# Optimization experiments

Hardware: AMD Instinct MI355X
Metric: run time of the kernel (lower is better)

## Reference

```python
import jax, jax.numpy as jnp
import numpy as np

B, S = 32, 128
VIDEO_SIZE, TITLE_SIZE = 768, 768
NUM_TAG, NUM_VOCAB, HIDDEN = 10000, 21128, 256


def setup_inputs() -> dict:
    key = jax.random.key(0)
    ks = jax.random.split(key, 10)
    video_feature = jax.random.normal(ks[0], (B, VIDEO_SIZE), dtype=jnp.float32)
    title_feature = jax.random.normal(ks[1], (B, S, TITLE_SIZE), dtype=jnp.float32)
    label_tag = jax.random.uniform(ks[2], (B, NUM_TAG), dtype=jnp.float32)
    label_mlm = jax.random.randint(ks[3], (B, S), 0, NUM_VOCAB, dtype=jnp.int64)
    Wt = jax.random.normal(ks[4], (NUM_TAG, VIDEO_SIZE), dtype=jnp.float32) * 0.02
    bt = jnp.zeros((NUM_TAG,), dtype=jnp.float32)
    Wm = jax.random.normal(ks[5], (NUM_VOCAB, TITLE_SIZE), dtype=jnp.float32) * 0.02
    bm = jnp.zeros((NUM_VOCAB,), dtype=jnp.float32)
    Wh = jax.random.normal(ks[6], (HIDDEN, VIDEO_SIZE + TITLE_SIZE), dtype=jnp.float32) * 0.02
    bh = jnp.zeros((HIDDEN,), dtype=jnp.float32)
    return {
        "video_feature": video_feature,
        "title_feature": title_feature,
        "label_tag": label_tag,
        "label_mlm": label_mlm,
        "Wt": Wt, "bt": bt, "Wm": Wm, "bm": bm, "Wh": Wh, "bh": bh,
    }


def reference(video_feature, title_feature, label_tag, label_mlm, Wt, bt, Wm, bm, Wh, bh):
    # tag head + BCEWithLogits (mean reduction), numerically stable form
    pred_tag = video_feature @ Wt.T + bt                       # [B, NUM_TAG]
    loss_tag = jnp.mean(
        jnp.maximum(pred_tag, 0.0) - pred_tag * label_tag
        + jnp.log1p(jnp.exp(-jnp.abs(pred_tag)))
    )
    pred_tag_sig = jax.nn.sigmoid(pred_tag)

    # mlm head: per-token vocab logits, masked CE summed over nonzero labels
    logits = jnp.einsum('bsd,vd->bsv', title_feature, Wm) + bm  # [B, S, V]
    lse = jax.nn.logsumexp(logits, axis=-1)                     # [B, S]
    gold = jnp.take_along_axis(logits, label_mlm[..., None], axis=-1)[..., 0]
    ce = lse - gold                                             # per-token NLL
    mask = (label_mlm != 0)
    loss_mlm = jnp.sum(jnp.where(mask, ce, 0.0))

    # fused embedding head + L2 normalize (torch eps 1e-12)
    feature = jnp.concatenate([video_feature, title_feature[:, 0]], axis=1)
    embedding = feature @ Wh.T + bh                             # [B, HIDDEN]
    norm = jnp.linalg.norm(embedding, axis=1, keepdims=True)
    normed_embedding = embedding / jnp.maximum(norm, 1e-12)

    return (pred_tag_sig, normed_embedding, loss_tag, loss_mlm)
```

## Files before the change

kernel.cpp:

```cpp
#include <hip/hip_runtime.h>
#include <hip/hip_bf16.h>
#include <math.h>

typedef short bf16x8 __attribute__((ext_vector_type(8)));
typedef float f32x4 __attribute__((ext_vector_type(4)));

#define KDIM 768
#define NTAG 10000
#define NVOC 21128
#define HID 256
#define NTOK 4096
#define NCHUNK 24
#define CHUNK 881
#define NTILE 56
#define M0 4.0f
#define WMSCALE 16.0f
#define INVSCALE 0.0625f
#define LOG2E 1.44269504f

#define WS_A     0ull
#define WS_AVID  3145728ull
#define WS_PSUM  3194880ull
#define WS_GOLD  3588096ull
#define WS_TAGL  3604480ull
#define WS_WM8   3604544ull
#define WS_NEED  (WS_WM8 + 16226304ull + 65536ull)

#define OUT_EMB  320000
#define OUT_LTAG 328192
#define OUT_LMLM 328193

#define TAG_BLKS 313
#define GOLD_BLKS 1024
#define EMB_BLKS 32

typedef const __attribute__((address_space(1))) unsigned int glds_g;
typedef __attribute__((address_space(3))) unsigned int glds_l;

static __device__ __forceinline__ unsigned short f2bf(float f) {
  unsigned u = __builtin_bit_cast(unsigned, f);
  u = u + 0x7FFFu + ((u >> 16) & 1u);
  return (unsigned short)(u >> 16);
}

static __device__ __forceinline__ int pk4_fp8(float4 v, float scale) {
  int w = __builtin_amdgcn_cvt_pk_fp8_f32(v.x * scale, v.y * scale, 0, false);
  w = __builtin_amdgcn_cvt_pk_fp8_f32(v.z * scale, v.w * scale, w, true);
  return w;
}

__global__ __launch_bounds__(256) void k_conv(
    const float* __restrict__ title, const float* __restrict__ video,
    const float* __restrict__ Wm,
    char* __restrict__ A8, unsigned short* __restrict__ Avid,
    char* __restrict__ Wm8, float* __restrict__ tagSum) {
  const int nT = 393216;
  const int nV = 3072;
  const int nW = 2028288;
  int i = blockIdx.x * 256 + threadIdx.x;
  if (i == 0) tagSum[0] = 0.f;
  if (i < nT) {
    float4 v0 = ((const float4*)title)[i * 2];
    float4 v1 = ((const float4*)title)[i * 2 + 1];
    int2 o = {pk4_fp8(v0, 1.f), pk4_fp8(v1, 1.f)};
    *(int2*)(A8 + (size_t)i * 8) = o;
  } else if (i < nT + nV) {
    int j = i - nT;
    float4 v0 = ((const float4*)video)[j * 2];
    float4 v1 = ((const float4*)video)[j * 2 + 1];
    bf16x8 o;
    o[0] = (short)f2bf(v0.x); o[1] = (short)f2bf(v0.y);
    o[2] = (short)f2bf(v0.z); o[3] = (short)f2bf(v0.w);
    o[4] = (short)f2bf(v1.x); o[5] = (short)f2bf(v1.y);
    o[6] = (short)f2bf(v1.z); o[7] = (short)f2bf(v1.w);
    *(bf16x8*)(Avid + (size_t)j * 8) = o;
  } else {
    int j = i - nT - nV;
    if (j >= nW) return;
    float4 v0 = ((const float4*)Wm)[j * 2];
    float4 v1 = ((const float4*)Wm)[j * 2 + 1];
    int2 o = {pk4_fp8(v0, WMSCALE), pk4_fp8(v1, WMSCALE)};
    *(int2*)(Wm8 + (size_t)j * 8) = o;
  }
}

template<bool WM8>
__global__ __launch_bounds__(256)
__attribute__((amdgpu_waves_per_eu(3, 3)))
void k_mlm(
    const char* __restrict__ A8,
    const float* __restrict__ Wm,
    const char* __restrict__ Wm8,
    const float* __restrict__ bm,
    float* __restrict__ psum) {
  __shared__ __align__(1024) char Bsm[2][12288];
  __shared__ float biasS[NTILE * 16];
  const int tid = threadIdx.x;
  const int lane = tid & 63, g = lane >> 4, col = lane & 15;
  const int wave = tid >> 6;
  const int chunk = blockIdx.x % NCHUNK, mt = blockIdx.x / NCHUNK;
  const int nbeg = chunk * CHUNK;
  const int nend = min(nbeg + CHUNK, NVOC);

  for (int i = tid; i < NTILE * 16; i += 256) {
    int n = nbeg + i;
    biasS[i] = (n < nend) ? (bm[n] - M0) * LOG2E : -1e30f;
  }

  const int arow0 = mt * 128 + wave * 32;
  long a0[24], a1[24];
  #pragma unroll
  for (int kk = 0; kk < 24; ++kk) {
    a0[kk] = *(const long*)(A8 + (size_t)(arow0 + col) * KDIM + kk * 32 + g * 8);
    a1[kk] = *(const long*)(A8 + (size_t)(arow0 + 16 + col) * KDIM + kk * 32 + g * 8);
  }

  float s[8];
  #pragma unroll
  for (int i = 0; i < 8; ++i) s[i] = 0.f;

  int e[3];
  #pragma unroll
  for (int j = 0; j < 3; ++j) {
    int sg = j * 256 + tid;
    int kk2 = sg >> 6, nl = (sg >> 2) & 15, q = sg & 3;
    int qp = q ^ ((nl >> 1) & 3);
    e[j] = nl * KDIM + kk2 * 64 + qp * 16;
  }

  const int off0 = col * 64 + ((g * 8) ^ (((col >> 1) & 3) << 4));
  const float kinv = INVSCALE * LOG2E;

  auto COMPUTE = [&](int t) {
    const char* Bb = &Bsm[t & 1][0];
    const char* B0 = Bb + off0;
    const char* B1 = Bb + (off0 ^ 32);
    f32x4 acc0 = {0.f, 0.f, 0.f, 0.f}, acc1 = {0.f, 0.f, 0.f, 0.f};
    #pragma unroll
    for (int kk = 0; kk < 24; ++kk) {
      long b = *(const long*)(((kk & 1) ? B1 : B0) + (kk >> 1) * 1024);
      acc0 = __builtin_amdgcn_mfma_f32_16x16x32_fp8_fp8(a0[kk], b, acc0, 0, 0, 0);
      acc1 = __builtin_amdgcn_mfma_f32_16x16x32_fp8_fp8(a1[kk], b, acc1, 0, 0, 0);
    }
    const float bias2 = biasS[t * 16 + col];
    #pragma unroll
    for (int rr = 0; rr < 4; ++rr) {
      s[rr]     += exp2f(fmaf(acc0[rr], kinv, bias2));
      s[rr + 4] += exp2f(fmaf(acc1[rr], kinv, bias2));
    }
  };

  if constexpr (WM8) {
    auto STAGE = [&](int buf, int tt) {
      const char* src = Wm8 + (size_t)(nbeg + tt * 16) * KDIM;
      char* dst = &Bsm[buf][0] + wave * 1024;
      #pragma unroll
      for (int j = 0; j < 3; ++j) {
        __builtin_amdgcn_global_load_lds((glds_g*)(src + e[j]),
                                         (glds_l*)(dst + j * 4096), 16, 0, 0);
      }
    };
    STAGE(0, 0);
    asm volatile("s_waitcnt lgkmcnt(0)" ::: "memory");
    __builtin_amdgcn_s_barrier();
    for (int t = 0; t < NTILE; ++t) {
      int tn = (t + 1 < NTILE) ? t + 1 : 0;
      STAGE((t + 1) & 1, tn);
      asm volatile("s_waitcnt vmcnt(3)" ::: "memory");
      __builtin_amdgcn_s_barrier();
      __builtin_amdgcn_sched_barrier(0);
      __builtin_amdgcn_s_setprio(1);
      COMPUTE(t);
      __builtin_amdgcn_s_setprio(0);
      __builtin_amdgcn_sched_barrier(0);
      __builtin_amdgcn_s_barrier();
    }
  } else {
    __syncthreads();
    for (int t = 0; t < NTILE; ++t) {
      #pragma unroll
      for (int j = 0; j < 3; ++j) {
        int sg = j * 256 + tid;
        int n = nbeg + t * 16 + ((sg >> 2) & 15);
        int kk2 = sg >> 6, q = sg & 3;
        int qp = q ^ ((((sg >> 2) & 15) >> 1) & 3);
        int koff = kk2 * 64 + qp * 16;
        int4 o = {0, 0, 0, 0};
        if (n < NVOC) {
          const float* wp = Wm + (size_t)n * KDIM + koff;
          float4 f0 = ((const float4*)wp)[0], f1 = ((const float4*)wp)[1];
          float4 f2 = ((const float4*)wp)[2], f3 = ((const float4*)wp)[3];
          o.x = pk4_fp8(f0, WMSCALE); o.y = pk4_fp8(f1, WMSCALE);
          o.z = pk4_fp8(f2, WMSCALE); o.w = pk4_fp8(f3, WMSCALE);
        }
        *(int4*)(&Bsm[0][0] + sg * 16) = o;
      }
      __syncthreads();
      COMPUTE(t);
      __syncthreads();
    }
  }

  #pragma unroll
  for (int i = 0; i < 8; ++i) {
    float v = s[i];
    v += __shfl_xor(v, 1);
    v += __shfl_xor(v, 2);
    v += __shfl_xor(v, 4);
    v += __shfl_xor(v, 8);
    s[i] = v;
  }
  if (col == 0) {
    #pragma unroll
    for (int mblk = 0; mblk < 2; ++mblk)
      #pragma unroll
      for (int rr = 0; rr < 4; ++rr) {
        int tok = arow0 + mblk * 16 + g * 4 + rr;
        psum[tok * NCHUNK + chunk] = s[mblk * 4 + rr];
      }
  }
}

__global__ __launch_bounds__(256) void k_tail(
    const unsigned short* __restrict__ Avid,
    const float* __restrict__ Wt, const float* __restrict__ bt,
    const float* __restrict__ ylab,
    const float* __restrict__ title, const int* __restrict__ lab,
    const float* __restrict__ Wm, const float* __restrict__ bm,
    const float* __restrict__ video,
    const float* __restrict__ Wh, const float* __restrict__ bh,
    float* __restrict__ out_sig, float* __restrict__ tagSum,
    float* __restrict__ gold, float* __restrict__ out_emb) {
  __shared__ __align__(1024) char smem[49664];
  const int bid = blockIdx.x, tid = threadIdx.x;
  const int wave = tid >> 6, lane = tid & 63, g = lane >> 4, col = lane & 15;

  if (bid < TAG_BLKS) {
    unsigned short* Bt = (unsigned short*)smem;
    float* wsum = (float*)(smem + 49152);
    #pragma unroll
    for (int j = 0; j < 12; ++j) {
      int sg = j * 256 + tid;
      int tt = (j >= 6) ? 1 : 0;
      int sgl = sg - tt * 1536;
      int kk = sgl >> 6, c = (sgl & 63) >> 2, gg = sgl & 3;
      int n = (bid * 2 + tt) * 16 + c;
      bf16x8 o = {};
      if (n < NTAG) {
        const float* wp = Wt + (size_t)n * KDIM + kk * 32 + gg * 8;
        float4 f0 = ((const float4*)wp)[0], f1 = ((const float4*)wp)[1];
        o[0] = (short)f2bf(f0.x); o[1] = (short)f2bf(f0.y);
        o[2] = (short)f2bf(f0.z); o[3] = (short)f2bf(f0.w);
        o[4] = (short)f2bf(f1.x); o[5] = (short)f2bf(f1.y);
        o[6] = (short)f2bf(f1.z); o[7] = (short)f2bf(f1.w);
      }
      *(bf16x8*)((char*)Bt + sg * 16) = o;
    }
    __syncthreads();

    const int ntile = bid * 2 + (wave >> 1), mhalf = wave & 1;
    float lacc = 0.f;
    if (ntile < 625) {
      bf16x8 a[24];
      #pragma unroll
      for (int kk = 0; kk < 24; ++kk)
        a[kk] = *(const bf16x8*)(Avid + (size_t)(mhalf * 16 + col) * KDIM + kk * 32 + g * 8);
      const char* Bb = (const char*)Bt + (wave >> 1) * 24576 + col * 64 + g * 16;
      f32x4 acc = {0.f, 0.f, 0.f, 0.f};
      #pragma unroll
      for (int kk = 0; kk < 24; ++kk) {
        bf16x8 b = *(const bf16x8*)(Bb + kk * 1024);
        acc = __builtin_amdgcn_mfma_f32_16x16x32_bf16(a[kk], b, acc, 0, 0, 0);
      }
      const int nc = ntile * 16 + col;
      if (nc < NTAG) {
        const float bias = bt[nc];
        #pragma unroll
        for (int rr = 0; rr < 4; ++rr) {
          int brow = mhalf * 16 + g * 4 + rr;
          float x = acc[rr] + bias;
          out_sig[(size_t)brow * NTAG + nc] = 1.f / (1.f + __expf(-x));
          float y = ylab[(size_t)brow * NTAG + nc];
          lacc += fmaxf(x, 0.f) - x * y + log1pf(__expf(-fabsf(x)));
        }
      }
    }
    #pragma unroll
    for (int m = 32; m; m >>= 1) lacc += __shfl_xor(lacc, m);
    if (lane == 0) wsum[wave] = lacc;
    __syncthreads();
    if (tid == 0) atomicAdd(tagSum, wsum[0] + wsum[1] + wsum[2] + wsum[3]);

  } else if (bid < TAG_BLKS + GOLD_BLKS) {
    int tok = (bid - TAG_BLKS) * 4 + wave;
    int l = lab[tok];
    float acc = 0.f;
    #pragma unroll
    for (int j = 0; j < 12; ++j) {
      int k = j * 64 + lane;
      acc += title[(size_t)tok * KDIM + k] * Wm[(size_t)l * KDIM + k];
    }
    #pragma unroll
    for (int m = 32; m; m >>= 1) acc += __shfl_xor(acc, m);
    if (lane == 0) gold[tok] = acc + bm[l];

  } else {
    float* feat = (float*)smem;
    float* red = (float*)(smem + 49152);
    const int b = bid - TAG_BLKS - GOLD_BLKS;
    #pragma unroll
    for (int j = 0; j < 6; ++j) {
      int k = j * 256 + tid;
      feat[k] = (k < KDIM) ? video[(size_t)b * KDIM + k]
                           : title[(size_t)b * 128 * KDIM + (k - KDIM)];
    }
    __syncthreads();
    float acc = bh[tid];
    #pragma unroll 8
    for (int k = 0; k < 1536; k += 4) {
      float4 w = *(const float4*)(Wh + (size_t)tid * 1536 + k);
      acc += w.x * feat[k] + w.y * feat[k + 1] + w.z * feat[k + 2] + w.w * feat[k + 3];
    }
    float ss = acc * acc;
    #pragma unroll
    for (int m = 32; m; m >>= 1) ss += __shfl_xor(ss, m);
    if (lane == 0) red[wave] = ss;
    __syncthreads();
    float nrm = sqrtf(red[0] + red[1] + red[2] + red[3]);
    float scale = 1.f / fmaxf(nrm, 1e-12f);
    out_emb[(size_t)b * HID + tid] = acc * scale;
  }
}

__global__ __launch_bounds__(256) void k_final(
    const float* __restrict__ psum, const float* __restrict__ gold,
    const int* __restrict__ lab, const float* __restrict__ tagSum,
    float* __restrict__ out) {
  __shared__ float red[4];
  const int tid = threadIdx.x, wave = tid >> 6, lane = tid & 63;
  if (tid == 0) out[OUT_LTAG] = tagSum[0] / 320000.f;

  float lm = 0.f;
  for (int tok = tid; tok < NTOK; tok += 256) {
    float S = 0.f;
    #pragma unroll
    for (int c = 0; c < NCHUNK; ++c) S += psum[tok * NCHUNK + c];
    float lse = M0 + logf(S);
    if (lab[tok] != 0) lm += lse - gold[tok];
  }
  #pragma unroll
  for (int m = 32; m; m >>= 1) lm += __shfl_xor(lm, m);
  if (lane == 0) red[wave] = lm;
  __syncthreads();
  if (tid == 0) out[OUT_LMLM] = red[0] + red[1] + red[2] + red[3];
}

extern "C" void kernel_launch(void* const* d_in, const int* in_sizes, int n_in,
                              void* d_out, int out_size, void* d_ws, size_t ws_size,
                              hipStream_t stream) {
  const float* video = (const float*)d_in[0];
  const float* title = (const float*)d_in[1];
  const float* ylab  = (const float*)d_in[2];
  const int*   lab   = (const int*)d_in[3];
  const float* Wt = (const float*)d_in[4];
  const float* bt = (const float*)d_in[5];
  const float* Wm = (const float*)d_in[6];
  const float* bm = (const float*)d_in[7];
  const float* Wh = (const float*)d_in[8];
  const float* bh = (const float*)d_in[9];
  float* out = (float*)d_out;
  char* ws = (char*)d_ws;

  char* wsA8   = ws + WS_A;
  unsigned short* wsAvid = (unsigned short*)(ws + WS_AVID);
  float* wsPsum = (float*)(ws + WS_PSUM);
  float* wsGold = (float*)(ws + WS_GOLD);
  float* wsTagl = (float*)(ws + WS_TAGL);
  char* wsWm8  = ws + WS_WM8;

  const bool useWm8 = ws_size >= WS_NEED;

  k_conv<<<9471, 256, 0, stream>>>(title, video, Wm, wsA8, wsAvid, wsWm8, wsTagl);
  if (useWm8)
    k_mlm<true><<<768, 256, 0, stream>>>(wsA8, Wm, wsWm8, bm, wsPsum);
  else
    k_mlm<false><<<768, 256, 0, stream>>>(wsA8, Wm, wsWm8, bm, wsPsum);
  k_tail<<<TAG_BLKS + GOLD_BLKS + EMB_BLKS, 256, 0, stream>>>(
      wsAvid, Wt, bt, ylab, title, lab, Wm, bm, video, Wh, bh,
      out, wsTagl, wsGold, out + OUT_EMB);
  k_final<<<1, 256, 0, stream>>>(wsPsum, wsGold, lab, wsTagl, out);
}
```

Baseline: 188.1 us.

## Pre-tile fp8 Wm into MFMA-fragment order in a separate conversion kernel

Moves the Wm fp32->fp8 conversion out of k_conv into a dedicated kernel that writes each 16-row vocab tile contiguously, in the exact fragment order the MFMA B-operand reads, with zero padding at chunk ends. k_mlm then stages each tile with fully contiguous global_load_lds copies and reads B with simple strided LDS offsets, so the XOR swizzle and the strided per-row gathers go away. The intent is more coalesced staging loads and simpler addressing in the hot loop. The cost is one extra kernel launch, slightly more workspace for padding, and a possible change in LDS bank-conflict behaviour since the swizzle is removed.

```diff
diff --git a/kernel.cpp b/kernel.cpp
--- a/kernel.cpp
+++ b/kernel.cpp
@@ -13,6 +13,7 @@
 #define NCHUNK 24
 #define CHUNK 881
 #define NTILE 56
+#define TILEB 12288
 #define M0 4.0f
 #define WMSCALE 16.0f
 #define INVSCALE 0.0625f
@@ -24,7 +25,7 @@
 #define WS_GOLD  3588096ull
 #define WS_TAGL  3604480ull
 #define WS_WM8   3604544ull
-#define WS_NEED  (WS_WM8 + 16226304ull + 65536ull)
+#define WS_NEED  (WS_WM8 + 16515072ull + 65536ull)
 
 #define OUT_EMB  320000
 #define OUT_LTAG 328192
@@ -51,12 +52,10 @@
 
 __global__ __launch_bounds__(256) void k_conv(
     const float* __restrict__ title, const float* __restrict__ video,
-    const float* __restrict__ Wm,
     char* __restrict__ A8, unsigned short* __restrict__ Avid,
-    char* __restrict__ Wm8, float* __restrict__ tagSum) {
+    float* __restrict__ tagSum) {
   const int nT = 393216;
   const int nV = 3072;
-  const int nW = 2028288;
   int i = blockIdx.x * 256 + threadIdx.x;
   if (i == 0) tagSum[0] = 0.f;
   if (i < nT) {
@@ -74,13 +73,29 @@
     o[4] = (short)f2bf(v1.x); o[5] = (short)f2bf(v1.y);
     o[6] = (short)f2bf(v1.z); o[7] = (short)f2bf(v1.w);
     *(bf16x8*)(Avid + (size_t)j * 8) = o;
-  } else {
-    int j = i - nT - nV;
-    if (j >= nW) return;
-    float4 v0 = ((const float4*)Wm)[j * 2];
-    float4 v1 = ((const float4*)Wm)[j * 2 + 1];
-    int2 o = {pk4_fp8(v0, WMSCALE), pk4_fp8(v1, WMSCALE)};
-    *(int2*)(Wm8 + (size_t)j * 8) = o;
+  }
+}
+
+__global__ __launch_bounds__(256) void k_convwm(
+    const float* __restrict__ Wm, char* __restrict__ Wm8) {
+  const int blk = blockIdx.x, tid = threadIdx.x;
+  const int chunk = blk / NTILE, tile = blk % NTILE;
+  const int n0 = chunk * CHUNK + tile * 16;
+  const int nend = min(chunk * CHUNK + CHUNK, NVOC);
+  char* dst = Wm8 + (size_t)blk * TILEB;
+  #pragma unroll
+  for (int j = 0; j < 6; ++j) {
+    int piece = j * 256 + tid;
+    int kk = piece >> 6, g = (piece >> 4) & 3, nl = piece & 15;
+    int n = n0 + nl;
+    int2 o = {0, 0};
+    if (n < nend) {
+      const float* wp = Wm + (size_t)n * KDIM + kk * 32 + g * 8;
+      float4 f0 = ((const float4*)wp)[0], f1 = ((const float4*)wp)[1];
+      o.x = pk4_fp8(f0, WMSCALE);
+      o.y = pk4_fp8(f1, WMSCALE);
+    }
+    *(int2*)(dst + piece * 8) = o;
   }
 }
 
@@ -93,7 +108,7 @@
     const char* __restrict__ Wm8,
     const float* __restrict__ bm,
     float* __restrict__ psum) {
-  __shared__ __align__(1024) char Bsm[2][12288];
+  __shared__ __align__(1024) char Bsm[2][TILEB];
   __shared__ float biasS[NTILE * 16];
   const int tid = threadIdx.x;
   const int lane = tid & 63, g = lane >> 4, col = lane & 15;
@@ -119,26 +134,15 @@
   #pragma unroll
   for (int i = 0; i < 8; ++i) s[i] = 0.f;
 
-  int e[3];
-  #pragma unroll
-  for (int j = 0; j < 3; ++j) {
-    int sg = j * 256 + tid;
-    int kk2 = sg >> 6, nl = (sg >> 2) & 15, q = sg & 3;
-    int qp = q ^ ((nl >> 1) & 3);
-    e[j] = nl * KDIM + kk2 * 64 + qp * 16;
-  }
-
-  const int off0 = col * 64 + ((g * 8) ^ (((col >> 1) & 3) << 4));
+  const int off0 = col * 8 + g * 128;
   const float kinv = INVSCALE * LOG2E;
 
   auto COMPUTE = [&](int t) {
-    const char* Bb = &Bsm[t & 1][0];
-    const char* B0 = Bb + off0;
-    const char* B1 = Bb + (off0 ^ 32);
+    const char* B = &Bsm[t & 1][0] + off0;
     f32x4 acc0 = {0.f, 0.f, 0.f, 0.f}, acc1 = {0.f, 0.f, 0.f, 0.f};
     #pragma unroll
     for (int kk = 0; kk < 24; ++kk) {
-      long b = *(const long*)(((kk & 1) ? B1 : B0) + (kk >> 1) * 1024);
+      long b = *(const long*)(B + kk * 512);
       acc0 = __builtin_amdgcn_mfma_f32_16x16x32_fp8_fp8(a0[kk], b, acc0, 0, 0, 0);
       acc1 = __builtin_amdgcn_mfma_f32_16x16x32_fp8_fp8(a1[kk], b, acc1, 0, 0, 0);
     }
@@ -151,12 +155,13 @@
   };
 
   if constexpr (WM8) {
+    const char* cbase = Wm8 + (size_t)chunk * NTILE * TILEB;
     auto STAGE = [&](int buf, int tt) {
-      const char* src = Wm8 + (size_t)(nbeg + tt * 16) * KDIM;
+      const char* src = cbase + (size_t)tt * TILEB + (wave * 64 + lane) * 16;
       char* dst = &Bsm[buf][0] + wave * 1024;
       #pragma unroll
       for (int j = 0; j < 3; ++j) {
-        __builtin_amdgcn_global_load_lds((glds_g*)(src + e[j]),
+        __builtin_amdgcn_global_load_lds((glds_g*)(src + j * 4096),
                                          (glds_l*)(dst + j * 4096), 16, 0, 0);
       }
     };
@@ -181,17 +186,18 @@
       #pragma unroll
       for (int j = 0; j < 3; ++j) {
         int sg = j * 256 + tid;
-        int n = nbeg + t * 16 + ((sg >> 2) & 15);
-        int kk2 = sg >> 6, q = sg & 3;
-        int qp = q ^ ((((sg >> 2) & 15) >> 1) & 3);
-        int koff = kk2 * 64 + qp * 16;
+        int kk = sg >> 5, gg = (sg >> 3) & 3, nl0 = (sg & 7) * 2;
+        int n_a = nbeg + t * 16 + nl0, n_b = n_a + 1;
         int4 o = {0, 0, 0, 0};
-        if (n < NVOC) {
-          const float* wp = Wm + (size_t)n * KDIM + koff;
-          float4 f0 = ((const float4*)wp)[0], f1 = ((const float4*)wp)[1];
-          float4 f2 = ((const float4*)wp)[2], f3 = ((const float4*)wp)[3];
-          o.x = pk4_fp8(f0, WMSCALE); o.y = pk4_fp8(f1, WMSCALE);
-          o.z = pk4_fp8(f2, WMSCALE); o.w = pk4_fp8(f3, WMSCALE);
+        if (n_a < nend) {
+          const float* wp = Wm + (size_t)n_a * KDIM + kk * 32 + gg * 8;
+          o.x = pk4_fp8(((const float4*)wp)[0], WMSCALE);
+          o.y = pk4_fp8(((const float4*)wp)[1], WMSCALE);
+        }
+        if (n_b < nend) {
+          const float* wp = Wm + (size_t)n_b * KDIM + kk * 32 + gg * 8;
+          o.z = pk4_fp8(((const float4*)wp)[0], WMSCALE);
+          o.w = pk4_fp8(((const float4*)wp)[1], WMSCALE);
         }
         *(int4*)(&Bsm[0][0] + sg * 16) = o;
       }
@@ -380,11 +386,13 @@
 
   const bool useWm8 = ws_size >= WS_NEED;
 
-  k_conv<<<9471, 256, 0, stream>>>(title, video, Wm, wsA8, wsAvid, wsWm8, wsTagl);
-  if (useWm8)
+  k_conv<<<1549, 256, 0, stream>>>(title, video, wsA8, wsAvid, wsTagl);
+  if (useWm8) {
+    k_convwm<<<NCHUNK * NTILE, 256, 0, stream>>>(Wm, wsWm8);
     k_mlm<true><<<768, 256, 0, stream>>>(wsA8, Wm, wsWm8, bm, wsPsum);
-  else
+  } else {
     k_mlm<false><<<768, 256, 0, stream>>>(wsA8, Wm, wsWm8, bm, wsPsum);
+  }
   k_tail<<<TAG_BLKS + GOLD_BLKS + EMB_BLKS, 256, 0, stream>>>(
       wsAvid, Wt, bt, ylab, title, lab, Wm, bm, video, Wh, bh,
       out, wsTagl, wsGold, out + OUT_EMB);
```

Result: slower. 194.2 us (+3.2%).
